# Kernel tuning notes

Hardware: AMD Instinct MI355X
Metric: run time of the kernel (lower is better)

The kernel has to match this reference:

```python
import jax, jax.numpy as jnp
import numpy as np


def setup_inputs() -> dict:
    key = jax.random.key(0)
    ks = jax.random.split(key, 9)
    B, T, D, H = 64, 512, 512, 512
    inp = {
        "x": jax.random.normal(ks[0], (B, T, D), dtype=jnp.float32),
        "W_c": jax.random.normal(ks[1], (D, H), dtype=jnp.float32) * 0.02,
        "W_i": jax.random.normal(ks[2], (D, H), dtype=jnp.float32) * 0.02,
        "W_f": jax.random.normal(ks[3], (D, H), dtype=jnp.float32) * 0.02,
        "W_o": jax.random.normal(ks[4], (D, H), dtype=jnp.float32) * 0.02,
        "U_c": jax.random.normal(ks[5], (H, H), dtype=jnp.float32) * 0.02,
        "U_i": jax.random.normal(ks[6], (H, H), dtype=jnp.float32) * 0.02,
        "U_f": jax.random.normal(ks[7], (H, H), dtype=jnp.float32) * 0.02,
        "U_o": jax.random.normal(ks[8], (H, H), dtype=jnp.float32) * 0.02,
        "b_c": jnp.zeros((H,), dtype=jnp.float32),
        "b_i": jnp.zeros((H,), dtype=jnp.float32),
        "b_f": jnp.zeros((H,), dtype=jnp.float32),
        "b_o": jnp.zeros((H,), dtype=jnp.float32),
    }
    return inp


def reference(x, W_c, W_i, W_f, W_o, U_c, U_i, U_f, U_o, b_c, b_i, b_f, b_o):
    # x: [B, T, D] -> scan over time-major [T, B, D]
    B, T, D = x.shape
    H = W_c.shape[1]
    h0 = jnp.zeros((B, H), dtype=x.dtype)
    c0 = jnp.zeros((B, H), dtype=x.dtype)

    # Precompute input projections for all timesteps (same math, hoisted
    # out of the recurrence since x does not depend on state).
    xt = jnp.transpose(x, (1, 0, 2))  # [T, B, D]
    xa = jnp.einsum('tbd,dh->tbh', xt, W_c) + b_c
    xi = jnp.einsum('tbd,dh->tbh', xt, W_i) + b_i
    xf = jnp.einsum('tbd,dh->tbh', xt, W_f) + b_f
    xo = jnp.einsum('tbd,dh->tbh', xt, W_o) + b_o

    def step(carry, elems):
        h, c = carry
        xa_t, xi_t, xf_t, xo_t = elems
        a = jnp.tanh(xa_t + h @ U_c)
        i = jax.nn.sigmoid(xi_t + h @ U_i)
        f = jax.nn.sigmoid(xf_t + h @ U_f)
        o = jax.nn.sigmoid(xo_t + h @ U_o)
        c_new = i * a + f * c
        h_new = o * jnp.tanh(c_new)
        return (h_new, c_new), h_new

    _, hs = jax.lax.scan(step, (h0, c0), (xa, xi, xf, xo))  # hs: [T, B, H]
    return jnp.transpose(hs, (1, 0, 2))  # return_sequence=True -> [B, T, H]
```

## Files before the change

kernel.cpp:

```cpp
#include <hip/hip_runtime.h>
#include <cstdint>
#include <cstddef>

typedef _Float16 half8  __attribute__((ext_vector_type(8)));
typedef float    floatx4 __attribute__((ext_vector_type(4)));
typedef unsigned long long ull;

#define B_  64
#define T_  512
#define D_  512
#define H_  512
#define NG  2048

static __device__ __forceinline__ float fast_sigmoid(float x) {
  return 1.0f / (1.0f + __expf(-x));
}
static __device__ __forceinline__ float fast_tanh(float x) {
  x = fminf(15.0f, fmaxf(-15.0f, x));
  float e = __expf(2.0f * x);
  return (e - 1.0f) / (e + 1.0f);
}

#define LDS_BARRIER() do {                                   \
    asm volatile("s_waitcnt lgkmcnt(0)" ::: "memory");       \
    __builtin_amdgcn_s_barrier();                            \
  } while (0)

#define TAGMASK 0x0000FFFF0000FFFFull

__global__ __launch_bounds__(256) void proj_kernel(
    const float* __restrict__ x,
    const float* __restrict__ Wc, const float* __restrict__ Wi,
    const float* __restrict__ Wf, const float* __restrict__ Wo,
    const float* __restrict__ bc, const float* __restrict__ bi,
    const float* __restrict__ bf2, const float* __restrict__ bo,
    _Float16* __restrict__ XG)
{
  const int tiles_n = NG / 64;
  int tM = blockIdx.x / tiles_n;
  int tN = blockIdx.x % tiles_n;
  int r0 = tM * 64;
  int t0 = r0 >> 6;
  int n0 = tN * 64;
  int g  = n0 >> 9;
  const float* W    = (g==0) ? Wc : (g==1) ? Wi : (g==2) ? Wf : Wo;
  const float* bias = (g==0) ? bc : (g==1) ? bi : (g==2) ? bf2 : bo;
  int j0 = n0 & (H_-1);

  __shared__ _Float16 Al[64*40];
  __shared__ _Float16 Bl[64*40];

  int tid  = threadIdx.x;
  int wave = tid >> 6;
  int lane = tid & 63;

  floatx4 acc[4] = {};

  int arow = tid >> 2;
  int ak0  = (tid & 3) * 8;
  const float* xsrc = x + ((size_t)arow * T_ + t0) * D_;

  int bcol = tid & 63;
  int bk0  = (tid >> 6) * 8;

  for (int k0 = 0; k0 < D_; k0 += 32) {
    half8 av;
    #pragma unroll
    for (int i = 0; i < 8; ++i) av[i] = (_Float16)xsrc[k0 + ak0 + i];
    *(half8*)&Al[arow*40 + ak0] = av;

    half8 bv;
    #pragma unroll
    for (int i = 0; i < 8; ++i)
      bv[i] = (_Float16)W[(size_t)(k0 + bk0 + i) * H_ + j0 + bcol];
    *(half8*)&Bl[bcol*40 + bk0] = bv;

    __syncthreads();

    half8 afrag = *(half8*)&Al[(wave*16 + (lane & 15))*40 + (lane >> 4)*8];
    #pragma unroll
    for (int ct = 0; ct < 4; ++ct) {
      half8 bfrag = *(half8*)&Bl[(ct*16 + (lane & 15))*40 + (lane >> 4)*8];
      acc[ct] = __builtin_amdgcn_mfma_f32_16x16x32_f16(afrag, bfrag, acc[ct], 0, 0, 0);
    }
    __syncthreads();
  }

  #pragma unroll
  for (int ct = 0; ct < 4; ++ct) {
    int col = n0 + ct*16 + (lane & 15);
    float bvs = bias[col & (H_-1)];
    #pragma unroll
    for (int i = 0; i < 4; ++i) {
      int row = r0 + wave*16 + (lane >> 4)*4 + i;
      XG[(size_t)row * NG + col] = (_Float16)(acc[ct][i] + bvs);
    }
  }
}

__global__ __launch_bounds__(256) void scan_kernel(
    const _Float16* __restrict__ XG,
    const float* __restrict__ Uc, const float* __restrict__ Ui,
    const float* __restrict__ Uf, const float* __restrict__ Uo,
    float* __restrict__ out, unsigned* __restrict__ dbuf)
{
  __shared__ _Float16 h_lds[16*512];

  int tid = threadIdx.x;
  int grp = blockIdx.x & 7;
  int member = blockIdx.x >> 3;

  int lane = tid & 63;
  int w    = tid >> 6;
  int c16  = lane & 15;
  int sub  = lane >> 4;
  int g    = c16 & 3;
  int jjl  = c16 >> 2;
  int jcol = member*16 + w*4 + jjl;
  int hi   = sub;
  bool pub = (g == 0) && (hi < 2);

  const float* Ug = (g==0) ? Uc : (g==1) ? Ui : (g==2) ? Uf : Uo;
  half8 uf[16];
  #pragma unroll
  for (int ks = 0; ks < 16; ++ks) {
    half8 v;
    #pragma unroll
    for (int q = 0; q < 8; ++q)
      v[q] = (_Float16)Ug[(size_t)(ks*32 + sub*8 + q) * H_ + jcol];
    uf[ks] = v;
  }

  int sm  = tid >> 3;
  int sb  = tid & 7;
  _Float16* stg = &h_lds[(sm >> 1)*512 + sb*32 + (sm & 1)*16];

  const _Float16* abase = &h_lds[c16*32 + sub*8];

  floatx4 c4 = {0.f, 0.f, 0.f, 0.f};
  float xg[4] = {0.f, 0.f, 0.f, 0.f};
  #pragma unroll
  for (int i = 0; i < 4; ++i)
    if (hi < 2)
      xg[i] = (float)XG[(size_t)(grp*8 + hi*4 + i) * NG + g*512 + jcol];

  for (int t = 0; t < T_; ++t) {
    LDS_BARRIER();

    {
      const ull* src8 = (const ull*)dbuf
          + ((size_t)(t & 1))*16384u + (size_t)grp*2048u + (size_t)tid*8u;
      ull want2 = (ull)(unsigned)(t & 0xFFFF) * 0x0000000100000001ull;
      ull w8[8];
      unsigned pend = 0xFFu;
      for (;;) {
        #pragma unroll
        for (int q = 0; q < 8; ++q)
          if (pend & (1u << q))
            w8[q] = __hip_atomic_load(src8 + q, __ATOMIC_RELAXED,
                                      __HIP_MEMORY_SCOPE_AGENT);
        unsigned npend = 0;
        #pragma unroll
        for (int q = 0; q < 8; ++q)
          if ((pend & (1u << q)) && ((w8[q] ^ want2) & TAGMASK))
            npend |= 1u << q;
        if (!npend) break;
        pend = npend;
        __builtin_amdgcn_s_sleep(2);
      }
      half8 hv0, hv1;
      #pragma unroll
      for (int q = 0; q < 4; ++q) {
        hv0[2*q]   = __builtin_bit_cast(_Float16, (unsigned short)((unsigned)w8[q]   >> 16));
        hv0[2*q+1] = __builtin_bit_cast(_Float16, (unsigned short)(w8[q]   >> 48));
        hv1[2*q]   = __builtin_bit_cast(_Float16, (unsigned short)((unsigned)w8[4+q] >> 16));
        hv1[2*q+1] = __builtin_bit_cast(_Float16, (unsigned short)(w8[4+q] >> 48));
      }
      *(half8*)stg       = hv0;
      *(half8*)(stg + 8) = hv1;
    }
    LDS_BARRIER();

    floatx4 a0 = {0.f,0.f,0.f,0.f}, a1 = {0.f,0.f,0.f,0.f};
    #pragma unroll
    for (int ks = 0; ks < 16; ks += 2) {
      half8 af0 = *(const half8*)(abase + ks*512);
      a0 = __builtin_amdgcn_mfma_f32_16x16x32_f16(af0, uf[ks],   a0, 0, 0, 0);
      half8 af1 = *(const half8*)(abase + (ks+1)*512);
      a1 = __builtin_amdgcn_mfma_f32_16x16x32_f16(af1, uf[ks+1], a1, 0, 0, 0);
    }

    float hval[4];
    #pragma unroll
    for (int i = 0; i < 4; ++i) {
      float pre = (a0[i] + a1[i]) + xg[i];
      float act = (g == 0) ? fast_tanh(pre) : fast_sigmoid(pre);
      float t1  = __shfl_xor(act, 1);
      float ia  = act * t1;
      float fv  = __shfl_xor(act, 2);
      float ov  = __shfl_xor(t1, 2);
      float cn  = fmaf(fv, c4[i], ia);
      c4[i] = cn;
      hval[i] = ov * fast_tanh(cn);
    }

    if (pub) {
      if (t + 1 < T_) {
        #pragma unroll
        for (int i = 0; i < 4; ++i) {
          unsigned wv = ((unsigned)__builtin_bit_cast(unsigned short,
                              (_Float16)hval[i]) << 16)
                      | ((unsigned)(t + 1) & 0xFFFFu);
          unsigned widx = ((unsigned)((t + 1) & 1))*32768u + (unsigned)grp*4096u
                        + (unsigned)member*128u
                        + (unsigned)((hi*4 + i)*16 + w*4 + jjl);
          __hip_atomic_store(&dbuf[widx], wv,
                             __ATOMIC_RELAXED, __HIP_MEMORY_SCOPE_AGENT);
        }
      }
      #pragma unroll
      for (int i = 0; i < 4; ++i)
        out[((size_t)(grp*8 + hi*4 + i) * T_ + t) * H_ + jcol] = hval[i];
    }

    if (t + 1 < T_) {
      #pragma unroll
      for (int i = 0; i < 4; ++i)
        if (hi < 2)
          xg[i] = (float)XG[((size_t)(t + 1)*B_ + grp*8 + hi*4 + i) * NG
                            + g*512 + jcol];
    }
  }
}

extern "C" void kernel_launch(void* const* d_in, const int* in_sizes, int n_in,
                              void* d_out, int out_size, void* d_ws, size_t ws_size,
                              hipStream_t stream)
{
  const float* x  = (const float*)d_in[0];
  const float* Wc = (const float*)d_in[1];
  const float* Wi = (const float*)d_in[2];
  const float* Wf = (const float*)d_in[3];
  const float* Wo = (const float*)d_in[4];
  const float* Uc = (const float*)d_in[5];
  const float* Ui = (const float*)d_in[6];
  const float* Uf = (const float*)d_in[7];
  const float* Uo = (const float*)d_in[8];
  const float* bc = (const float*)d_in[9];
  const float* bi = (const float*)d_in[10];
  const float* bf2= (const float*)d_in[11];
  const float* bo = (const float*)d_in[12];
  float* out = (float*)d_out;

  const size_t XG_BYTES = (size_t)T_ * B_ * NG * sizeof(_Float16);
  const size_t DB_BYTES = (size_t)2 * 8 * 4096 * sizeof(unsigned);

  if (ws_size < XG_BYTES + DB_BYTES) return;

  _Float16* XG   = (_Float16*)d_ws;
  unsigned* dbuf = (unsigned*)((char*)d_ws + XG_BYTES);

  (void)hipMemsetAsync(dbuf, 0, DB_BYTES, stream);

  proj_kernel<<<dim3((T_*B_/64) * (NG/64)), dim3(256), 0, stream>>>(
      x, Wc, Wi, Wf, Wo, bc, bi, bf2, bo, XG);

  scan_kernel<<<dim3(256), dim3(256), 0, stream>>>(
      XG, Uc, Ui, Uf, Uo, out, dbuf);
}
```

Baseline: 2.060 ms.

## Double-buffer spin polling, pad LDS h tile, publish h values earlier

```diff
diff --git a/kernel.cpp b/kernel.cpp
--- a/kernel.cpp
+++ b/kernel.cpp
@@ -27,6 +27,17 @@
   } while (0)
 
 #define TAGMASK 0x0000FFFF0000FFFFull
+
+static __device__ __forceinline__ void unpack16(const ull* w8,
+                                                half8& hv0, half8& hv1) {
+  #pragma unroll
+  for (int q = 0; q < 4; ++q) {
+    hv0[2*q]   = __builtin_bit_cast(_Float16, (unsigned short)((unsigned)w8[q]   >> 16));
+    hv0[2*q+1] = __builtin_bit_cast(_Float16, (unsigned short)(w8[q]   >> 48));
+    hv1[2*q]   = __builtin_bit_cast(_Float16, (unsigned short)((unsigned)w8[4+q] >> 16));
+    hv1[2*q+1] = __builtin_bit_cast(_Float16, (unsigned short)(w8[4+q] >> 48));
+  }
+}
 
 __global__ __launch_bounds__(256) void proj_kernel(
     const float* __restrict__ x,
@@ -104,7 +115,7 @@
     const float* __restrict__ Uf, const float* __restrict__ Uo,
     float* __restrict__ out, unsigned* __restrict__ dbuf)
 {
-  __shared__ _Float16 h_lds[16*512];
+  __shared__ _Float16 h_lds[16*640];
 
   int tid = threadIdx.x;
   int grp = blockIdx.x & 7;
@@ -133,9 +144,9 @@
 
   int sm  = tid >> 3;
   int sb  = tid & 7;
-  _Float16* stg = &h_lds[(sm >> 1)*512 + sb*32 + (sm & 1)*16];
-
-  const _Float16* abase = &h_lds[c16*32 + sub*8];
+  _Float16* stg = &h_lds[(sm >> 1)*640 + sb*40 + (sm & 1)*16];
+
+  const _Float16* abase = &h_lds[c16*40 + sub*8];
 
   floatx4 c4 = {0.f, 0.f, 0.f, 0.f};
   float xg[4] = {0.f, 0.f, 0.f, 0.f};
@@ -151,30 +162,30 @@
       const ull* src8 = (const ull*)dbuf
           + ((size_t)(t & 1))*16384u + (size_t)grp*2048u + (size_t)tid*8u;
       ull want2 = (ull)(unsigned)(t & 0xFFFF) * 0x0000000100000001ull;
-      ull w8[8];
-      unsigned pend = 0xFFu;
-      for (;;) {
-        #pragma unroll
-        for (int q = 0; q < 8; ++q)
-          if (pend & (1u << q))
-            w8[q] = __hip_atomic_load(src8 + q, __ATOMIC_RELAXED,
-                                      __HIP_MEMORY_SCOPE_AGENT);
-        unsigned npend = 0;
-        #pragma unroll
-        for (int q = 0; q < 8; ++q)
-          if ((pend & (1u << q)) && ((w8[q] ^ want2) & TAGMASK))
-            npend |= 1u << q;
-        if (!npend) break;
-        pend = npend;
-        __builtin_amdgcn_s_sleep(2);
-      }
+      ull wA[8], wB[8];
       half8 hv0, hv1;
       #pragma unroll
-      for (int q = 0; q < 4; ++q) {
-        hv0[2*q]   = __builtin_bit_cast(_Float16, (unsigned short)((unsigned)w8[q]   >> 16));
-        hv0[2*q+1] = __builtin_bit_cast(_Float16, (unsigned short)(w8[q]   >> 48));
-        hv1[2*q]   = __builtin_bit_cast(_Float16, (unsigned short)((unsigned)w8[4+q] >> 16));
-        hv1[2*q+1] = __builtin_bit_cast(_Float16, (unsigned short)(w8[4+q] >> 48));
+      for (int q = 0; q < 8; ++q)
+        wA[q] = __hip_atomic_load(src8 + q, __ATOMIC_RELAXED,
+                                  __HIP_MEMORY_SCOPE_AGENT);
+      for (;;) {
+        #pragma unroll
+        for (int q = 0; q < 8; ++q)
+          wB[q] = __hip_atomic_load(src8 + q, __ATOMIC_RELAXED,
+                                    __HIP_MEMORY_SCOPE_AGENT);
+        ull diff = 0;
+        #pragma unroll
+        for (int q = 0; q < 8; ++q) diff |= (wA[q] ^ want2) & TAGMASK;
+        if (!diff) { unpack16(wA, hv0, hv1); break; }
+        #pragma unroll
+        for (int q = 0; q < 8; ++q)
+          wA[q] = __hip_atomic_load(src8 + q, __ATOMIC_RELAXED,
+                                    __HIP_MEMORY_SCOPE_AGENT);
+        diff = 0;
+        #pragma unroll
+        for (int q = 0; q < 8; ++q) diff |= (wB[q] ^ want2) & TAGMASK;
+        if (!diff) { unpack16(wB, hv0, hv1); break; }
+        __builtin_amdgcn_s_sleep(1);
       }
       *(half8*)stg       = hv0;
       *(half8*)(stg + 8) = hv1;
@@ -184,9 +195,9 @@
     floatx4 a0 = {0.f,0.f,0.f,0.f}, a1 = {0.f,0.f,0.f,0.f};
     #pragma unroll
     for (int ks = 0; ks < 16; ks += 2) {
-      half8 af0 = *(const half8*)(abase + ks*512);
+      half8 af0 = *(const half8*)(abase + ks*640);
       a0 = __builtin_amdgcn_mfma_f32_16x16x32_f16(af0, uf[ks],   a0, 0, 0, 0);
-      half8 af1 = *(const half8*)(abase + (ks+1)*512);
+      half8 af1 = *(const half8*)(abase + (ks+1)*640);
       a1 = __builtin_amdgcn_mfma_f32_16x16x32_f16(af1, uf[ks+1], a1, 0, 0, 0);
     }
 
@@ -201,23 +212,21 @@
       float ov  = __shfl_xor(t1, 2);
       float cn  = fmaf(fv, c4[i], ia);
       c4[i] = cn;
-      hval[i] = ov * fast_tanh(cn);
+      float hv = ov * fast_tanh(cn);
+      hval[i] = hv;
+      if (pub && (t + 1 < T_)) {
+        unsigned wv = ((unsigned)__builtin_bit_cast(unsigned short,
+                            (_Float16)hv) << 16)
+                    | ((unsigned)(t + 1) & 0xFFFFu);
+        unsigned widx = ((unsigned)((t + 1) & 1))*32768u + (unsigned)grp*4096u
+                      + (unsigned)member*128u
+                      + (unsigned)((hi*4 + i)*16 + w*4 + jjl);
+        __hip_atomic_store(&dbuf[widx], wv,
+                           __ATOMIC_RELAXED, __HIP_MEMORY_SCOPE_AGENT);
+      }
     }
 
     if (pub) {
-      if (t + 1 < T_) {
-        #pragma unroll
-        for (int i = 0; i < 4; ++i) {
-          unsigned wv = ((unsigned)__builtin_bit_cast(unsigned short,
-                              (_Float16)hval[i]) << 16)
-                      | ((unsigned)(t + 1) & 0xFFFFu);
-          unsigned widx = ((unsigned)((t + 1) & 1))*32768u + (unsigned)grp*4096u
-                        + (unsigned)member*128u
-                        + (unsigned)((hi*4 + i)*16 + w*4 + jjl);
-          __hip_atomic_store(&dbuf[widx], wv,
-                             __ATOMIC_RELAXED, __HIP_MEMORY_SCOPE_AGENT);
-        }
-      }
       #pragma unroll
       for (int i = 0; i < 4; ++i)
         out[((size_t)(grp*8 + hi*4 + i) * T_ + t) * H_ + jcol] = hval[i];
```

Result: slower. 2.442 ms (+18.5%).
